# Kernel optimization log

Hardware: AMD Instinct MI355X
Metric: run time of the kernel (lower is better)

The kernel has to match this reference:

```python
import jax, jax.numpy as jnp
import numpy as np

EPS_BN = 1e-5

def _grid_sample(fea, gx, gy):
    # fea: [B,C,H,W]; gx,gy: [B,P] normalized to [-1,1]; bilinear, zeros padding, align_corners=True
    B, C, H, W = fea.shape
    x = (gx + 1.0) * 0.5 * (W - 1)
    y = (gy + 1.0) * 0.5 * (H - 1)
    x0 = jnp.floor(x)
    y0 = jnp.floor(y)
    wx1 = x - x0
    wy1 = y - y0
    flat = fea.reshape(B, C, H * W)
    def tap(xi, yi, w):
        valid = ((xi >= 0) & (xi <= W - 1) & (yi >= 0) & (yi <= H - 1)).astype(fea.dtype)
        xi_c = jnp.clip(xi, 0, W - 1).astype(jnp.int32)
        yi_c = jnp.clip(yi, 0, H - 1).astype(jnp.int32)
        g = jnp.take_along_axis(flat, (yi_c * W + xi_c)[:, None, :], axis=2)  # [B,C,P]
        return g * (w * valid)[:, None, :]
    return (tap(x0, y0, (1 - wx1) * (1 - wy1)) + tap(x0 + 1, y0, wx1 * (1 - wy1))
            + tap(x0, y0 + 1, (1 - wx1) * wy1) + tap(x0 + 1, y0 + 1, wx1 * wy1))

def _homo_warp(src_fea, src_proj, ref_proj, depth_values):
    # src_fea: [B,C,H,W] -> warped [B,C,D,H,W] (MVSNet homo_warping, grid under stop_gradient)
    B, C, H, W = src_fea.shape
    D = depth_values.shape[1]
    proj = jnp.matmul(src_proj, jnp.linalg.inv(ref_proj))
    rot, trans = proj[:, :3, :3], proj[:, :3, 3]
    yy, xx = jnp.meshgrid(jnp.arange(H, dtype=src_fea.dtype), jnp.arange(W, dtype=src_fea.dtype), indexing='ij')
    xyz = jnp.stack([xx.ravel(), yy.ravel(), jnp.ones(H * W, src_fea.dtype)], 0)  # [3,HW]
    rot_xyz = jnp.einsum('bij,jp->bip', rot, xyz)  # [B,3,HW]
    pxyz = rot_xyz[:, :, None, :] * depth_values.reshape(B, 1, D, H * W) + trans[:, :, None, None]  # [B,3,D,HW]
    z = pxyz[:, 2]
    gx = jax.lax.stop_gradient(((pxyz[:, 0] / z) / ((W - 1) / 2.0) - 1.0).reshape(B, D * H * W))
    gy = jax.lax.stop_gradient(((pxyz[:, 1] / z) / ((H - 1) / 2.0) - 1.0).reshape(B, D * H * W))
    return _grid_sample(src_fea, gx, gy).reshape(B, C, D, H, W)

def _pixelwise_net(x, w0, g0, b0, m0, v0, w1, g1, b1, m1, v1, w2, b2):
    # x: [B,1,D,H,W]; 1x1x1 Conv3d(bias=False)+BN+ReLU twice, then Conv3d(8->1)+sigmoid+max over D
    def bnrelu(h, g, b, m, v):
        s = (1, -1, 1, 1, 1)
        return jax.nn.relu((h - m.reshape(s)) * (g / jnp.sqrt(v + EPS_BN)).reshape(s) + b.reshape(s))
    h = bnrelu(jnp.einsum('oc,bcdhw->bodhw', w0, x), g0, b0, m0, v0)
    h = bnrelu(jnp.einsum('oc,bcdhw->bodhw', w1, h), g1, b1, m1, v1)
    h = jnp.einsum('oc,bcdhw->bodhw', w2, h) + b2.reshape(1, -1, 1, 1, 1)
    out = jax.nn.sigmoid(h[:, 0])  # [B,D,H,W]
    return jnp.max(out, axis=1, keepdims=True)  # [B,1,H,W]

def _forward(features, proj_matrices, depth_values, num_depth,
             pw_w0, pw_g0, pw_b0, pw_m0, pw_v0, pw_w1, pw_g1, pw_b1, pw_m1, pw_v1, pw_w2, pw_b2,
             reg_w, reg_b):
    ref_fea = features[0]
    B, C, H, W = ref_fea.shape
    V = features.shape[0]
    D = num_depth
    def proj_new(p):  # p: [B,2,4,4] -> K @ E on top 3 rows
        top = jnp.matmul(p[:, 1, :3, :3], p[:, 0, :3, :4])
        return jnp.concatenate([top, p[:, 0, 3:4, :]], axis=1)
    ref_proj_new = proj_new(proj_matrices[:, 0])
    sim_sum = jnp.zeros((B, 1, D, H, W), ref_fea.dtype)
    w_sum = jnp.full((B, 1, 1, H, W), 1e-5, ref_fea.dtype)
    vw_list = []
    for i in range(1, V):  # small fixed loop over source views
        src_proj_new = proj_new(proj_matrices[:, i])
        warped = _homo_warp(features[i], src_proj_new, ref_proj_new, depth_values)
        sim = jnp.mean(warped * ref_fea[:, :, None], axis=1, keepdims=True)  # [B,1,D,H,W]
        vw = _pixelwise_net(sim, pw_w0, pw_g0, pw_b0, pw_m0, pw_v0, pw_w1, pw_g1, pw_b1, pw_m1, pw_v1, pw_w2, pw_b2)
        vw_list.append(vw)
        sim_sum = sim_sum + sim * vw[:, :, None]
        w_sum = w_sum + vw[:, :, None]
    similarity = sim_sum / w_sum
    cost_reg = jax.lax.conv_general_dilated(similarity, reg_w, (1, 1, 1), 'SAME',
                                            dimension_numbers=('NCDHW', 'OIDHW', 'NCDHW')) + reg_b.reshape(1, -1, 1, 1, 1)
    prob_volume = jax.nn.softmax(cost_reg[:, 0], axis=1)  # exp(log_softmax) == softmax
    idx = jnp.argmax(prob_volume, axis=1, keepdims=True)
    depth = jnp.take_along_axis(depth_values, idx, axis=1)[:, 0]  # WTA depth [B,H,W]
    conf = jnp.max(prob_volume, axis=1)
    view_weights = jnp.concatenate(vw_list, axis=1)
    return depth, conf, prob_volume, cost_reg, view_weights

def setup_inputs():
    key = jax.random.key(0)
    ks = jax.random.split(key, 20)
    B, V, C, H, W, D = 2, 5, 32, 128, 160, 32
    features = jax.random.normal(ks[0], (V, B, C, H, W), jnp.float32)
    K = np.eye(4, dtype=np.float32)
    K[0, 0] = 180.0; K[1, 1] = 180.0; K[0, 2] = W / 2.0; K[1, 2] = H / 2.0
    pm = np.zeros((B, V, 2, 4, 4), np.float32)
    for v in range(V):
        E = np.eye(4, dtype=np.float32)
        E[0, 3] = 10.0 * v  # horizontal baseline per source view
        pm[:, v, 0] = E
        pm[:, v, 1] = K
    depth_values = jnp.broadcast_to(jnp.linspace(425.0, 935.0, D, dtype=jnp.float32)[None, :, None, None], (B, D, H, W)) + 0.0
    rn = lambda k, s, sc=0.3: jax.random.normal(k, s, jnp.float32) * sc
    return {
        'features': features,
        'proj_matrices': jnp.asarray(pm),
        'depth_values': depth_values,
        'num_depth': D,
        'pw_w0': rn(ks[1], (16, 1)),
        'pw_g0': 1.0 + rn(ks[2], (16,), 0.1), 'pw_b0': rn(ks[3], (16,), 0.1),
        'pw_m0': rn(ks[4], (16,), 0.1), 'pw_v0': 1.0 + 0.5 * jax.random.uniform(ks[5], (16,)),
        'pw_w1': rn(ks[6], (8, 16)),
        'pw_g1': 1.0 + rn(ks[7], (8,), 0.1), 'pw_b1': rn(ks[8], (8,), 0.1),
        'pw_m1': rn(ks[9], (8,), 0.1), 'pw_v1': 1.0 + 0.5 * jax.random.uniform(ks[10], (8,)),
        'pw_w2': rn(ks[11], (1, 8)),
        'pw_b2': rn(ks[12], (1,), 0.1),
        'reg_w': rn(ks[13], (1, 1, 3, 3, 3), 0.1),
        'reg_b': rn(ks[14], (1,), 0.1),
    }

def reference(features, proj_matrices, depth_values, num_depth,
              pw_w0, pw_g0, pw_b0, pw_m0, pw_v0, pw_w1, pw_g1, pw_b1, pw_m1, pw_v1, pw_w2, pw_b2,
              reg_w, reg_b):
    return _forward(features, proj_matrices, depth_values, num_depth,
                    pw_w0, pw_g0, pw_b0, pw_m0, pw_v0, pw_w1, pw_g1, pw_b1, pw_m1, pw_v1, pw_w2, pw_b2,
                    reg_w, reg_b)
```

## Files before the change

### kernel.cpp

```cpp
#include <hip/hip_runtime.h>
#include <math.h>

#define BB 2
#define VV 5
#define CC 32
#define HH 128
#define WW 160
#define DD 32
#define HWp (HH*WW)
#define NV (VV-1)
#define PX 16
#define MAXSLOT 18

#define OFF_RT   0
#define OFF_PRM  96
#define OFF_FEAT 512
#define OFF_SIM  (OFF_FEAT + VV*BB*HWp*CC)
#define OFF_T    (OFF_SIM + BB*DD*HWp)
#define OFF_TAB  (OFF_T + 16)
#define OFF_FLAG (OFF_TAB + 17*16)

#define OUT_DEPTH 0
#define OUT_CONF  (BB*HWp)
#define OUT_PROB  (2*BB*HWp)
#define OUT_COST  (OUT_PROB + BB*DD*HWp)
#define OUT_VW    (OUT_COST + BB*DD*HWp)

#define ZI(d,k)     smemU[(d)*17 + (k)]
#define DEP(d,k)    smemU[(d)*17 + (k)]
#define REF(p,c)    smemU[544 + (p)*36 + (c)]
#define GT(v,p,i)   smemU[1120 + ((v)*16 + (p))*18 + (i)]
#define AY0(v,p)    smemU[2272 + (v)*16 + (p)]
#define AY1(v,p)    smemU[2336 + (v)*16 + (p)]
#define IR0(v,p)    smemI[2400 + (v)*16 + (p)]
#define IR1(v,p)    smemI[2464 + (v)*16 + (p)]
#define IXB(v,p)    smemI[2528 + (v)*16 + (p)]
#define ISL(v,p)    smemI[2592 + (v)*16 + (p)]
#define BADF        smemI[2656]
#define SIMG(v,d,p) smemU[544 + (((v)*32 + (d))*17 + (p))]

__device__ void build_proj(const float* proj, int b, int v, double M[4][4]) {
    const float* E = proj + (((b*VV + v)*2 + 0)*16);
    const float* K = proj + (((b*VV + v)*2 + 1)*16);
    for (int r = 0; r < 3; r++)
        for (int c = 0; c < 4; c++) {
            double s = 0.0;
            for (int k = 0; k < 3; k++) s += (double)K[r*4+k] * (double)E[k*4+c];
            M[r][c] = s;
        }
    for (int c = 0; c < 4; c++) M[3][c] = (double)E[12+c];
}

__device__ void inv4(const double M[4][4], double out[4][4]) {
    double a[4][8];
    for (int i = 0; i < 4; i++)
        for (int j = 0; j < 4; j++) { a[i][j] = M[i][j]; a[i][4+j] = (i == j) ? 1.0 : 0.0; }
    for (int col = 0; col < 4; col++) {
        int piv = col; double best = fabs(a[col][col]);
        for (int r = col+1; r < 4; r++) if (fabs(a[r][col]) > best) { best = fabs(a[r][col]); piv = r; }
        if (piv != col) for (int j = 0; j < 8; j++) { double t = a[col][j]; a[col][j] = a[piv][j]; a[piv][j] = t; }
        double dinv = 1.0 / a[col][col];
        for (int j = 0; j < 8; j++) a[col][j] *= dinv;
        for (int r = 0; r < 4; r++) {
            if (r == col) continue;
            double f = a[r][col];
            for (int j = 0; j < 8; j++) a[r][j] -= f * a[col][j];
        }
    }
    for (int i = 0; i < 4; i++) for (int j = 0; j < 4; j++) out[i][j] = a[i][4+j];
}

__device__ void setup_body(const float* __restrict__ proj,
    const float* __restrict__ w0, const float* __restrict__ g0, const float* __restrict__ b0,
    const float* __restrict__ m0, const float* __restrict__ v0,
    const float* __restrict__ w1, const float* __restrict__ g1, const float* __restrict__ b1,
    const float* __restrict__ m1, const float* __restrict__ v1,
    const float* __restrict__ w2, const float* __restrict__ b2,
    float* __restrict__ ws, int t,
    float* __restrict__ prmL, float* __restrict__ TL) {

    if (t < BB*NV) {
        int b = t / NV, v = 1 + (t % NV);
        double refM[4][4], inv[4][4], S[4][4];
        build_proj(proj, b, 0, refM);
        inv4(refM, inv);
        build_proj(proj, b, v, S);
        float* rt = ws + OFF_RT + (b*NV + (v-1))*12;
        for (int r = 0; r < 3; r++) {
            for (int c = 0; c < 3; c++) {
                double s = 0.0;
                for (int k = 0; k < 4; k++) s += S[r][k] * inv[k][c];
                rt[r*3 + c] = (float)s;
            }
            double s = 0.0;
            for (int k = 0; k < 4; k++) s += S[r][k] * inv[k][3];
            rt[9 + r] = (float)s;
        }
    }

    if (t < 16) {
        float sc = g0[t] / sqrtf(v0[t] + 1e-5f);
        prmL[t]      = w0[t] * sc;
        prmL[16 + t] = b0[t] - m0[t] * sc;
    }
    if (t >= 32 && t < 160) {
        int i = t - 32, q = i >> 4, o = i & 15;
        float sc = g1[q] / sqrtf(v1[q] + 1e-5f);
        prmL[32 + q*16 + o] = w1[q*16 + o] * sc;
    }
    if (t >= 160 && t < 168) {
        int q = t - 160;
        float sc = g1[q] / sqrtf(v1[q] + 1e-5f);
        prmL[160 + q] = b1[q] - m1[q] * sc;
        prmL[168 + q] = w2[q];
    }
    if (t == 176) prmL[176] = b2[0];
    __syncthreads();

    if (t < BB) {
        int ok = 1;
        for (int i = 0; i < NV; i++) {
            const float* ri = ws + OFF_RT + (t*NV + i)*12;
            ok &= (fabsf(ri[6])        < 1e-6f);
            ok &= (fabsf(ri[7])        < 1e-6f);
            ok &= (fabsf(ri[8] - 1.f)  < 1e-6f);
            ok &= (fabsf(ri[10])       < 1e-6f);
            ok &= (fabsf(ri[11])       < 1e-6f);
        }
        ws[OFF_FLAG + t] = ok ? 1.f : 0.f;
    }

    if (t == 0) {
        float tmp[16]; int nk = 0;
        for (int o = 0; o < 16; o++) {
            float a = prmL[o];
            if (a != 0.f) tmp[nk++] = -prmL[16+o] / a;
        }
        for (int i = 1; i < nk; i++) {
            float key = tmp[i]; int j = i-1;
            while (j >= 0 && tmp[j] > key) { tmp[j+1] = tmp[j]; j--; }
            tmp[j+1] = key;
        }
        for (int i = 0; i < 16; i++) TL[i] = (i < nk) ? tmp[i] : 3.4e38f;
    }
    __syncthreads();

    if (t < 17*8) {
        int seg = t >> 3, q = t & 7;
        float lo = (seg == 0)  ? -1e30f : TL[seg-1];
        float hi = (seg == 16) ?  1e30f : TL[seg];
        float smid;
        if (hi > 1e29f)       smid = lo + 1.f;
        else if (lo < -1e29f) smid = hi - 1.f;
        else                  smid = 0.5f*(lo + hi);
        float alpha = 0.f, beta = prmL[160+q];
        #pragma unroll
        for (int o = 0; o < 16; o++) {
            float a = prmL[o], c = prmL[16+o];
            if (a*smid + c > 0.f) {
                alpha += prmL[32+q*16+o]*a;
                beta  += prmL[32+q*16+o]*c;
            }
        }
        ws[OFF_TAB + seg*16 + q]     = alpha;
        ws[OFF_TAB + seg*16 + 8 + q] = beta;
    }
    if (t < 177) ws[OFF_PRM + t] = prmL[t];
    if (t < 16)  ws[OFF_T + t]   = TL[t];
}

__global__ __launch_bounds__(256) void transpose_setup_kernel(
    const float* __restrict__ fea, float* __restrict__ featT,
    const float* __restrict__ proj,
    const float* __restrict__ w0, const float* __restrict__ g0, const float* __restrict__ b0,
    const float* __restrict__ m0, const float* __restrict__ v0,
    const float* __restrict__ w1, const float* __restrict__ g1, const float* __restrict__ b1,
    const float* __restrict__ m1, const float* __restrict__ v1,
    const float* __restrict__ w2, const float* __restrict__ b2,
    float* __restrict__ ws) {
    __shared__ float prmL[177];
    __shared__ float TL[16];
    if (blockIdx.x == 0)
        setup_body(proj, w0, g0, b0, m0, v0, w1, g1, b1, m1, v1, w2, b2,
                   ws, threadIdx.x, prmL, TL);

    int t = blockIdx.x*256 + threadIdx.x;
    int w = t % WW;
    int h = (t / WW) % HH;
    int b = (t / (WW*HH)) % BB;
    int v = t / (WW*HH*BB);
    const float* src = fea + (size_t)((v*BB + b)*CC) * HWp + h*WW + w;
    float* dst = featT + (size_t)((v*BB + b)*HWp + h*WW + w) * CC;
    #pragma unroll
    for (int c = 0; c < CC; c += 4) {
        float4 q;
        q.x = src[(c+0)*HWp];
        q.y = src[(c+1)*HWp];
        q.z = src[(c+2)*HWp];
        q.w = src[(c+3)*HWp];
        *reinterpret_cast<float4*>(dst + c) = q;
    }
}

__device__ __forceinline__ float half_max(float v) {
    v = fmaxf(v, __shfl_xor(v, 1));
    v = fmaxf(v, __shfl_xor(v, 2));
    v = fmaxf(v, __shfl_xor(v, 4));
    v = fmaxf(v, __shfl_xor(v, 8));
    v = fmaxf(v, __shfl_xor(v, 16));
    return v;
}

__device__ __forceinline__ float dot32(const float* __restrict__ col,
                                       const float* __restrict__ refp) {
    float acc = 0.f;
    #pragma unroll
    for (int c = 0; c < CC; c += 4) {
        float4 a = *reinterpret_cast<const float4*>(col + c);
        float4 r = *reinterpret_cast<const float4*>(refp + c);
        acc = fmaf(a.w, r.w, fmaf(a.z, r.z, fmaf(a.y, r.y, fmaf(a.x, r.x, acc))));
    }
    return acc;
}

__device__ __forceinline__ void mlp_out(
    float s0, float s1, float s2, float s3,
    int d2, int b, int p,
    const float* __restrict__ tabL, const float* __restrict__ Tg,
    const float* __restrict__ prm,
    float* __restrict__ out, float* __restrict__ simout) {
    float T0 = Tg[0], T1 = Tg[1], T2 = Tg[2], T3 = Tg[3];
    float T4 = Tg[4], T5 = Tg[5], T6 = Tg[6], T7 = Tg[7];
    float T8 = Tg[8], T9 = Tg[9], T10 = Tg[10], T11 = Tg[11];
    float T12 = Tg[12], T13 = Tg[13], T14 = Tg[14], T15 = Tg[15];
    float wq0 = prm[168], wq1 = prm[169], wq2 = prm[170], wq3 = prm[171];
    float wq4 = prm[172], wq5 = prm[173], wq6 = prm[174], wq7 = prm[175];
    float p176 = prm[176];

    float sv[NV] = {s0, s1, s2, s3};
    float vw[NV];
    #pragma unroll
    for (int v = 0; v < NV; v++) {
        float s = sv[v];
        int seg = 0;
        seg += (s > T0);  seg += (s > T1);  seg += (s > T2);  seg += (s > T3);
        seg += (s > T4);  seg += (s > T5);  seg += (s > T6);  seg += (s > T7);
        seg += (s > T8);  seg += (s > T9);  seg += (s > T10); seg += (s > T11);
        seg += (s > T12); seg += (s > T13); seg += (s > T14); seg += (s > T15);
        const float* row = &tabL[seg << 4];
        float4 A0 = *reinterpret_cast<const float4*>(row);
        float4 A1 = *reinterpret_cast<const float4*>(row + 4);
        float4 B0 = *reinterpret_cast<const float4*>(row + 8);
        float4 B1 = *reinterpret_cast<const float4*>(row + 12);
        float h2v = p176;
        h2v = fmaf(wq0, fmaxf(fmaf(A0.x, s, B0.x), 0.f), h2v);
        h2v = fmaf(wq1, fmaxf(fmaf(A0.y, s, B0.y), 0.f), h2v);
        h2v = fmaf(wq2, fmaxf(fmaf(A0.z, s, B0.z), 0.f), h2v);
        h2v = fmaf(wq3, fmaxf(fmaf(A0.w, s, B0.w), 0.f), h2v);
        h2v = fmaf(wq4, fmaxf(fmaf(A1.x, s, B1.x), 0.f), h2v);
        h2v = fmaf(wq5, fmaxf(fmaf(A1.y, s, B1.y), 0.f), h2v);
        h2v = fmaf(wq6, fmaxf(fmaf(A1.z, s, B1.z), 0.f), h2v);
        h2v = fmaf(wq7, fmaxf(fmaf(A1.w, s, B1.w), 0.f), h2v);
        float m = half_max(h2v);
        vw[v] = 1.f/(1.f + __expf(-m));
    }

    if (d2 == 0) out[OUT_VW + (b*NV + 0)*HWp + p] = vw[0];
    if (d2 == 1) out[OUT_VW + (b*NV + 1)*HWp + p] = vw[1];
    if (d2 == 2) out[OUT_VW + (b*NV + 2)*HWp + p] = vw[2];
    if (d2 == 3) out[OUT_VW + (b*NV + 3)*HWp + p] = vw[3];

    float wsum = 1e-5f + vw[0] + vw[1] + vw[2] + vw[3];
    float ssum = s0*vw[0] + s1*vw[1] + s2*vw[2] + s3*vw[3];
    simout[(b*DD + d2)*HWp + p] = ssum / wsum;
}

__device__ __forceinline__ float tap_blend(
    const float* __restrict__ vbv, int sub8, float sx,
    float ay0, float ay1, int r0, int r1,
    float4 rva, float4 rvb) {
    float x0f = floorf(sx);
    float wx1 = sx - x0f;
    float wx0 = 1.f - wx1;
    int xi0 = (int)x0f, xi1 = xi0 + 1;
    float ax0 = ((unsigned)xi0 < WW) ? wx0 : 0.f;
    float ax1 = ((unsigned)xi1 < WW) ? wx1 : 0.f;
    int xc0 = min(max(xi0, 0), WW-1);
    int xc1 = min(max(xi1, 0), WW-1);
    float w00 = ax0*ay0, w01 = ax1*ay0;
    const float* q00 = vbv + (((r0 + xc0) << 5) + sub8);
    const float* q01 = vbv + (((r0 + xc1) << 5) + sub8);
    float4 t00a = *reinterpret_cast<const float4*>(q00);
    float4 t00b = *reinterpret_cast<const float4*>(q00 + 4);
    float4 t01a = *reinterpret_cast<const float4*>(q01);
    float4 t01b = *reinterpret_cast<const float4*>(q01 + 4);

    float blx = fmaf(w01, t01a.x, w00*t00a.x);
    float bly = fmaf(w01, t01a.y, w00*t00a.y);
    float blz = fmaf(w01, t01a.z, w00*t00a.z);
    float blw = fmaf(w01, t01a.w, w00*t00a.w);
    float acc = fmaf(rva.w,blw, fmaf(rva.z,blz, fmaf(rva.y,bly, rva.x*blx)));
    blx = fmaf(w01, t01b.x, w00*t00b.x);
    bly = fmaf(w01, t01b.y, w00*t00b.y);
    blz = fmaf(w01, t01b.z, w00*t00b.z);
    blw = fmaf(w01, t01b.w, w00*t00b.w);
    acc = fmaf(rvb.w,blw, fmaf(rvb.z,blz, fmaf(rvb.y,bly, fmaf(rvb.x,blx, acc))));

    if (ay1 != 0.f) {
        float w10 = ax0*ay1, w11 = ax1*ay1;
        const float* q10 = vbv + (((r1 + xc0) << 5) + sub8);
        const float* q11 = vbv + (((r1 + xc1) << 5) + sub8);
        float4 t10a = *reinterpret_cast<const float4*>(q10);
        float4 t10b = *reinterpret_cast<const float4*>(q10 + 4);
        float4 t11a = *reinterpret_cast<const float4*>(q11);
        float4 t11b = *reinterpret_cast<const float4*>(q11 + 4);
        float cx = fmaf(w11, t11a.x, w10*t10a.x);
        float cy = fmaf(w11, t11a.y, w10*t10a.y);
        float cz = fmaf(w11, t11a.z, w10*t10a.z);
        float cw = fmaf(w11, t11a.w, w10*t10a.w);
        acc = fmaf(rva.w,cw, fmaf(rva.z,cz, fmaf(rva.y,cy, fmaf(rva.x,cx, acc))));
        cx = fmaf(w11, t11b.x, w10*t10b.x);
        cy = fmaf(w11, t11b.y, w10*t10b.y);
        cz = fmaf(w11, t11b.z, w10*t10b.z);
        cw = fmaf(w11, t11b.w, w10*t10b.w);
        acc = fmaf(rvb.w,cw, fmaf(rvb.z,cz, fmaf(rvb.y,cy, fmaf(rvb.x,cx, acc))));
    }
    return acc;
}

__global__ __launch_bounds__(256) void fused_sim_kernel(
    const float* __restrict__ featT, const float* __restrict__ rtAll,
    const float* __restrict__ prm, const float* __restrict__ Tg,
    const float* __restrict__ tabG, const float* __restrict__ flagG,
    const float* __restrict__ depthv,
    float* __restrict__ simout, float* __restrict__ out) {
    __shared__ __align__(16) float smemU[2720];
    __shared__ __align__(16) float tabL[17*16];
    int* smemI = (int*)smemU;

    int t = threadIdx.x;
    int b = blockIdx.y;
    int pbase = blockIdx.x * PX;
    int hi  = pbase / WW;
    int wi0 = pbase % WW;
    float fy = (float)hi;

    bool fast = (flagG[b] != 0.f);

    {
        int di = t >> 4, k = t & 15;
        float dep0 = depthv[(b*DD + di)*HWp + pbase + k];
        float dep1 = depthv[(b*DD + di + 16)*HWp + pbase + k];
        if (fast) {
            ZI(di, k)    = __builtin_amdgcn_rcpf(dep0);
            ZI(di+16, k) = __builtin_amdgcn_rcpf(dep1);
            if (t < 128) {
                int p = t >> 3, c4 = (t & 7) * 4;
                float4 rq = *reinterpret_cast<const float4*>(
                    featT + (size_t)(b*HWp + pbase + p)*CC + c4);
                *reinterpret_cast<float4*>(&REF(p, c4)) = rq;
            }
        } else {
            DEP(di, k)    = dep0;
            DEP(di+16, k) = dep1;
        }
        tabL[t] = tabG[t];
        if (t < 16) tabL[256 + t] = tabG[256 + t];
        if (t == 0 && fast) BADF = 0;
    }
    __syncthreads();

    float rc[NV][12];
    #pragma unroll
    for (int v = 0; v < NV; v++)
        #pragma unroll
        for (int j = 0; j < 12; j++)
            rc[v][j] = rtAll[(b*NV + v)*12 + j];
    float bx0[NV], by0[NV], bz0[NV];
    #pragma unroll
    for (int v = 0; v < NV; v++) {
        bx0[v] = fmaf((float)wi0, rc[v][0], fmaf(fy, rc[v][1], rc[v][2]));
        by0[v] = fmaf((float)wi0, rc[v][3], fmaf(fy, rc[v][4], rc[v][5]));
        bz0[v] = fmaf((float)wi0, rc[v][6], fmaf(fy, rc[v][7], rc[v][8]));
    }

    bool needRestage = false;
    if (fast) {
        int p_loc = t >> 5, d = t & 31;
        for (int ph = 0; ph < 2; ph++) {
            int p = ph*8 + p_loc;
            float zi = ZI(d, p);
            float mnz = zi, mxz = zi;
            #pragma unroll
            for (int off = 1; off <= 16; off <<= 1) {
                mnz = fminf(mnz, __shfl_xor(mnz, off));
                mxz = fmaxf(mxz, __shfl_xor(mxz, off));
            }
            if (d == 0) {
                float fk = (float)p;
                #pragma unroll
                for (int v = 0; v < NV; v++) {
                    float bx = fmaf(fk, rc[v][0], bx0[v]);
                    float t0c = rc[v][9];
                    float sxa = fmaf(t0c, mnz, bx);
                    float sxb = fmaf(t0c, mxz, bx);
                    float mn = fminf(sxa, sxb), mx = fmaxf(sxa, sxb);
                    float by = fmaf(fk, rc[v][3], by0[v]);
                    float sy = by;
                    float sny = rintf(sy);
                    sy = (fabsf(sy - sny) < 1e-4f) ? sny : sy;
                    float y0f = floorf(sy);
                    float wy1 = sy - y0f, wy0 = 1.f - wy1;
                    int yi0 = (int)y0f, yi1 = yi0 + 1;
                    AY0(v, p) = ((unsigned)yi0 < HH) ? wy0 : 0.f;
                    AY1(v, p) = ((unsigned)yi1 < HH) ? wy1 : 0.f;
                    IR0(v, p) = min(max(yi0, 0), HH-1)*WW;
                    IR1(v, p) = min(max(yi1, 0), HH-1)*WW;
                    bool finite = (mn > -1e9f) && (mx < 1e9f) && (mn == mn) && (mx == mx);
                    int xb = finite ? (int)floorf(mn) : 0;
                    int slots = finite ? ((int)floorf(mx) - xb + 2) : MAXSLOT + 1;
                    IXB(v, p) = xb;
                    ISL(v, p) = slots;
                    if (slots > MAXSLOT) BADF = 1;
                }
            }
        }
        __syncthreads();
        if (BADF) { fast = false; needRestage = true; }
    }

    if (fast) {
        {
            int v2 = t & 3, p2 = (t >> 2) & 15, i0 = t >> 6;
            float ay0 = AY0(v2, p2), ay1 = AY1(v2, p2);
            int r0 = IR0(v2, p2), r1 = IR1(v2, p2);
            int xb = IXB(v2, p2), slots = ISL(v2, p2);
            const float* vbv = featT + (size_t)(((v2+1)*BB + b)*HWp)*CC;
            const float* refp = &REF(p2, 0);
            for (int i2 = i0; i2 < slots; i2 += 4) {
                int xc = min(max(xb + i2, 0), WW-1);
                float g = ay0 * dot32(vbv + ((r0 + xc) << 5), refp);
                if (ay1 != 0.f) g = fmaf(ay1, dot32(vbv + ((r1 + xc) << 5), refp), g);
                GT(v2, p2, i2) = g * (1.f/(float)CC);
            }
        }
        __syncthreads();
        {
            int p_loc = t >> 5, d = t & 31;
            for (int ph = 0; ph < 2; ph++) {
                int p = ph*8 + p_loc;
                float fk = (float)p;
                float zi = ZI(d, p);
                float sv[NV];
                #pragma unroll
                for (int v = 0; v < NV; v++) {
                    float bx = fmaf(fk, rc[v][0], bx0[v]);
                    float sx = fmaf(rc[v][9], zi, bx);
                    float x0f = floorf(sx);
                    float wx1 = sx - x0f, wx0 = 1.f - wx1;
                    int xi0 = (int)x0f, xi1 = xi0 + 1;
                    float ax0 = ((unsigned)xi0 < WW) ? wx0 : 0.f;
                    float ax1 = ((unsigned)xi1 < WW) ? wx1 : 0.f;
                    int ii = xi0 - IXB(v, p);
                    float g0 = GT(v, p, ii);
                    float g1 = GT(v, p, ii+1);
                    sv[v] = fmaf(ax0, g0, ax1*g1);
                }
                mlp_out(sv[0], sv[1], sv[2], sv[3], d, b, pbase + p,
                        tabL, Tg, prm, out, simout);
            }
        }
        return;
    }

    if (needRestage) {
        int di = t >> 4, k = t & 15;
        DEP(di, k)    = depthv[(b*DD + di)*HWp + pbase + k];
        DEP(di+16, k) = depthv[(b*DD + di + 16)*HWp + pbase + k];
        __syncthreads();
    }
    {
        int sub = t & 3;
        int dB  = (t >> 2) & 31;
        int kk  = t >> 7;
        int sub8 = sub*8;
        #pragma unroll 2
        for (int j = 0; j < PX/2; j++) {
            int kpix = j*2 + kk;
            int p = pbase + kpix;
            float fk = (float)kpix;
            float depth = DEP(dB, kpix);
            const float* refp = featT + (size_t)(b*HWp + p)*CC + sub8;
            float4 rva = *reinterpret_cast<const float4*>(refp);
            float4 rvb = *reinterpret_cast<const float4*>(refp + 4);

            #pragma unroll
            for (int v = 0; v < NV; v++) {
                float bx = fmaf(fk, rc[v][0], bx0[v]);
                float by = fmaf(fk, rc[v][3], by0[v]);
                float bz = fmaf(fk, rc[v][6], bz0[v]);
                float px = fmaf(bx, depth, rc[v][9]);
                float py = fmaf(by, depth, rc[v][10]);
                float pz = fmaf(bz, depth, rc[v][11]);
                float zi = __builtin_amdgcn_rcpf(pz);
                float sx = px * zi, sy = py * zi;
                float sny = rintf(sy);
                sy = (fabsf(sy - sny) < 1e-4f) ? sny : sy;
                float y0f = floorf(sy);
                float wy1 = sy - y0f, wy0 = 1.f - wy1;
                int yi0 = (int)y0f, yi1 = yi0 + 1;
                float ay0 = ((unsigned)yi0 < HH) ? wy0 : 0.f;
                float ay1 = ((unsigned)yi1 < HH) ? wy1 : 0.f;
                int yc0 = min(max(yi0, 0), HH-1);
                int yc1 = min(max(yi1, 0), HH-1);
                int r0 = yc0*WW, r1 = yc1*WW;
                const float* vbv = featT + (size_t)(((v+1)*BB + b)*HWp)*CC;
                float acc = tap_blend(vbv, sub8, sx, ay0, ay1, r0, r1, rva, rvb);
                acc += __shfl_xor(acc, 1);
                acc += __shfl_xor(acc, 2);
                if (sub == 0) SIMG(v, dB, kpix) = acc * (1.f/(float)CC);
            }
        }
        __syncthreads();

        int p8 = t >> 5;
        int d2 = t & 31;
        #pragma unroll
        for (int pi = 0; pi < PX/8; pi++) {
            int pidx = pi*8 + p8;
            mlp_out(SIMG(0, d2, pidx), SIMG(1, d2, pidx),
                    SIMG(2, d2, pidx), SIMG(3, d2, pidx),
                    d2, b, pbase + pidx, tabL, Tg, prm, out, simout);
        }
    }
}

__global__ __launch_bounds__(256) void convsm_kernel(
    const float* __restrict__ sim, const float* __restrict__ rw,
    const float* __restrict__ rb, const float* __restrict__ depthv,
    float* __restrict__ out) {
    __shared__ float tile[34*121 + 7];
    int t = threadIdx.x;
    int tw = blockIdx.x * 8;
    int th = blockIdx.y * 8;
    int b  = blockIdx.z;

    for (int i = t; i < 34*120; i += 256) {
        int e = i / 120; int rem = i % 120;
        int h = rem / 12, w = rem % 12;
        int gd = e - 1, gh = th + h - 1, gw = tw + w - 1;
        float v = 0.f;
        if (w < 10 && gd >= 0 && gd < DD && (unsigned)gh < HH && (unsigned)gw < WW)
            v = sim[((b*DD + gd)*HH + gh)*WW + gw];
        tile[e*121 + rem] = v;
    }
    __syncthreads();

    float wk[27];
    #pragma unroll
    for (int i = 0; i < 27; i++) wk[i] = rw[i];
    float bias = rb[0];

    int p  = t >> 2, dq = t & 3;
    int ph = p >> 3, pw = p & 7;
    int d0 = dq * 8;

    float cost[8];
    #pragma unroll
    for (int j = 0; j < 8; j++) cost[j] = bias;
    #pragma unroll
    for (int e = 0; e < 10; e++) {
        int el = d0 + e;
        float s0 = 0.f, s1 = 0.f, s2 = 0.f;
        #pragma unroll
        for (int kh = 0; kh < 3; kh++) {
            #pragma unroll
            for (int kw = 0; kw < 3; kw++) {
                float x = tile[el*121 + (ph+kh)*12 + (pw+kw)];
                s0 = fmaf(wk[0*9 + kh*3 + kw], x, s0);
                s1 = fmaf(wk[1*9 + kh*3 + kw], x, s1);
                s2 = fmaf(wk[2*9 + kh*3 + kw], x, s2);
            }
        }
        if (e < 8)            cost[e]   += s0;
        if (e >= 1 && e <= 8) cost[e-1] += s1;
        if (e >= 2)           cost[e-2] += s2;
    }

    int pg = (th + ph)*WW + (tw + pw);
    #pragma unroll
    for (int j = 0; j < 8; j++)
        out[OUT_COST + (b*DD + d0 + j)*HWp + pg] = cost[j];

    float m = cost[0]; int mi = d0;
    #pragma unroll
    for (int j = 1; j < 8; j++) { if (cost[j] > m) { m = cost[j]; mi = d0 + j; } }
    #pragma unroll
    for (int off = 1; off <= 2; off <<= 1) {
        float m2 = __shfl_xor(m, off);
        int  i2 = __shfl_xor(mi, off);
        if (m2 > m || (m2 == m && i2 < mi)) { m = m2; mi = i2; }
    }
    float sum = 0.f;
    float e8[8];
    #pragma unroll
    for (int j = 0; j < 8; j++) { e8[j] = __expf(cost[j] - m); sum += e8[j]; }
    #pragma unroll
    for (int off = 1; off <= 2; off <<= 1) sum += __shfl_xor(sum, off);
    float inv = 1.f / sum;
    #pragma unroll
    for (int j = 0; j < 8; j++)
        out[OUT_PROB + (b*DD + d0 + j)*HWp + pg] = e8[j] * inv;
    if (dq == 0) {
        out[OUT_DEPTH + b*HWp + pg] = depthv[(b*DD + mi)*HWp + pg];
        out[OUT_CONF  + b*HWp + pg] = inv;
    }
}

extern "C" void kernel_launch(void* const* d_in, const int* in_sizes, int n_in,
                              void* d_out, int out_size, void* d_ws, size_t ws_size,
                              hipStream_t stream) {
    const float* features = (const float*)d_in[0];
    const float* proj     = (const float*)d_in[1];
    const float* depthv   = (const float*)d_in[2];
    const float* w0 = (const float*)d_in[4];
    const float* g0 = (const float*)d_in[5];
    const float* b0 = (const float*)d_in[6];
    const float* m0 = (const float*)d_in[7];
    const float* v0 = (const float*)d_in[8];
    const float* w1 = (const float*)d_in[9];
    const float* g1 = (const float*)d_in[10];
    const float* b1 = (const float*)d_in[11];
    const float* m1 = (const float*)d_in[12];
    const float* v1 = (const float*)d_in[13];
    const float* w2 = (const float*)d_in[14];
    const float* b2 = (const float*)d_in[15];
    const float* rw = (const float*)d_in[16];
    const float* rb = (const float*)d_in[17];
    float* out = (float*)d_out;
    float* ws  = (float*)d_ws;

    transpose_setup_kernel<<<VV*BB*HWp/256, 256, 0, stream>>>(
        features, ws + OFF_FEAT, proj,
        w0, g0, b0, m0, v0, w1, g1, b1, m1, v1, w2, b2, ws);

    fused_sim_kernel<<<dim3(HWp/PX, BB), 256, 0, stream>>>(
        ws + OFF_FEAT, ws + OFF_RT, ws + OFF_PRM, ws + OFF_T, ws + OFF_TAB,
        ws + OFF_FLAG, depthv, ws + OFF_SIM, out);

    convsm_kernel<<<dim3(WW/8, HH/8, BB), 256, 0, stream>>>(
        ws + OFF_SIM, rw, rb, depthv, out);
}
```

Before: 77.53 us.

## Stage shared source-view row segment in LDS when all pixels hit one row

Adds a uniform-row fast path. When every pixel in a block samples the same single source row per view (no second y tap), the union x-range of feature columns is loaded cooperatively into padded LDS once. The per-pixel dot products then read from LDS instead of issuing redundant global loads for overlapping columns. In exchange, LDS use per block grows by about 24KB, which may reduce occupancy, and an extra barrier and a reduction step are added.

```diff
diff --git a/kernel.cpp b/kernel.cpp
--- a/kernel.cpp
+++ b/kernel.cpp
@@ -11,6 +11,7 @@
 #define NV (VV-1)
 #define PX 16
 #define MAXSLOT 18
+#define UWMAX 44
 
 #define OFF_RT   0
 #define OFF_PRM  96
@@ -38,6 +39,10 @@
 #define ISL(v,p)    smemI[2592 + (v)*16 + (p)]
 #define BADF        smemI[2656]
 #define SIMG(v,d,p) smemU[544 + (((v)*32 + (d))*17 + (p))]
+#define COLU(v,ux,c) smemU[2720 + (v)*(UWMAX*33) + (ux)*33 + (c)]
+#define UOKI(v)     smemI[8528 + (v)]
+#define UXLOI(v)    smemI[8532 + (v)]
+#define UWI(v)      smemI[8536 + (v)]
 
 __device__ void build_proj(const float* proj, int b, int v, double M[4][4]) {
     const float* E = proj + (((b*VV + v)*2 + 0)*16);
@@ -219,6 +224,19 @@
         float4 a = *reinterpret_cast<const float4*>(col + c);
         float4 r = *reinterpret_cast<const float4*>(refp + c);
         acc = fmaf(a.w, r.w, fmaf(a.z, r.z, fmaf(a.y, r.y, fmaf(a.x, r.x, acc))));
+    }
+    return acc;
+}
+
+__device__ __forceinline__ float dot32_lds(const float* __restrict__ col,
+                                           const float* __restrict__ refp) {
+    float acc = 0.f;
+    #pragma unroll
+    for (int c = 0; c < CC; c += 4) {
+        acc = fmaf(col[c+3], refp[c+3],
+              fmaf(col[c+2], refp[c+2],
+              fmaf(col[c+1], refp[c+1],
+              fmaf(col[c+0], refp[c+0], acc))));
     }
     return acc;
 }
@@ -334,7 +352,7 @@
     const float* __restrict__ tabG, const float* __restrict__ flagG,
     const float* __restrict__ depthv,
     float* __restrict__ simout, float* __restrict__ out) {
-    __shared__ __align__(16) float smemU[2720];
+    __shared__ __align__(16) float smemU[8544];
     __shared__ __align__(16) float tabL[17*16];
     int* smemI = (int*)smemU;
 
@@ -429,22 +447,79 @@
         if (BADF) { fast = false; needRestage = true; }
     }
 
+    bool uni = false;
     if (fast) {
-        {
-            int v2 = t & 3, p2 = (t >> 2) & 15, i0 = t >> 6;
-            float ay0 = AY0(v2, p2), ay1 = AY1(v2, p2);
-            int r0 = IR0(v2, p2), r1 = IR1(v2, p2);
-            int xb = IXB(v2, p2), slots = ISL(v2, p2);
-            const float* vbv = featT + (size_t)(((v2+1)*BB + b)*HWp)*CC;
-            const float* refp = &REF(p2, 0);
-            for (int i2 = i0; i2 < slots; i2 += 4) {
-                int xc = min(max(xb + i2, 0), WW-1);
-                float g = ay0 * dot32(vbv + ((r0 + xc) << 5), refp);
-                if (ay1 != 0.f) g = fmaf(ay1, dot32(vbv + ((r1 + xc) << 5), refp), g);
-                GT(v2, p2, i2) = g * (1.f/(float)CC);
+        if (t < 64) {
+            int v = t >> 4, p = t & 15;
+            int ok = (AY1(v, p) == 0.f) && (IR0(v, p) == IR0(v, 0)) ? 1 : 0;
+            int xlo = IXB(v, p);
+            int xhi = xlo + ISL(v, p) - 1;
+            #pragma unroll
+            for (int off = 1; off <= 8; off <<= 1) {
+                ok  &= __shfl_xor(ok, off);
+                xlo  = min(xlo, __shfl_xor(xlo, off));
+                xhi  = max(xhi, __shfl_xor(xhi, off));
+            }
+            if (p == 0) {
+                int wdt = xhi - xlo + 1;
+                UOKI(v)  = (ok && wdt <= UWMAX) ? 1 : 0;
+                UXLOI(v) = xlo;
+                UWI(v)   = wdt;
             }
         }
         __syncthreads();
+        uni = UOKI(0) && UOKI(1) && UOKI(2) && UOKI(3);
+    }
+
+    if (fast) {
+        if (uni) {
+            for (int i = t; i < NV*UWMAX*8; i += 256) {
+                int v  = i / (UWMAX*8);
+                int rem = i - v*(UWMAX*8);
+                int ux = rem >> 3, c4 = (rem & 7) * 4;
+                if (ux < UWI(v)) {
+                    int xc = min(max(UXLOI(v) + ux, 0), WW-1);
+                    int r0 = IR0(v, 0);
+                    const float* src = featT + (size_t)(((v+1)*BB + b)*HWp)*CC
+                                       + ((r0 + xc) << 5) + c4;
+                    float4 q = *reinterpret_cast<const float4*>(src);
+                    COLU(v, ux, c4+0) = q.x;
+                    COLU(v, ux, c4+1) = q.y;
+                    COLU(v, ux, c4+2) = q.z;
+                    COLU(v, ux, c4+3) = q.w;
+                }
+            }
+            __syncthreads();
+            {
+                int v2 = t & 3, p2 = (t >> 2) & 15, i0 = t >> 6;
+                float ay0 = AY0(v2, p2);
+                int xb = IXB(v2, p2), slots = ISL(v2, p2);
+                int xoff = xb - UXLOI(v2);
+                const float* refp = &REF(p2, 0);
+                for (int i2 = i0; i2 < slots; i2 += 4) {
+                    const float* col = &COLU(v2, xoff + i2, 0);
+                    float g = ay0 * dot32_lds(col, refp);
+                    GT(v2, p2, i2) = g * (1.f/(float)CC);
+                }
+            }
+            __syncthreads();
+        } else {
+            {
+                int v2 = t & 3, p2 = (t >> 2) & 15, i0 = t >> 6;
+                float ay0 = AY0(v2, p2), ay1 = AY1(v2, p2);
+                int r0 = IR0(v2, p2), r1 = IR1(v2, p2);
+                int xb = IXB(v2, p2), slots = ISL(v2, p2);
+                const float* vbv = featT + (size_t)(((v2+1)*BB + b)*HWp)*CC;
+                const float* refp = &REF(p2, 0);
+                for (int i2 = i0; i2 < slots; i2 += 4) {
+                    int xc = min(max(xb + i2, 0), WW-1);
+                    float g = ay0 * dot32(vbv + ((r0 + xc) << 5), refp);
+                    if (ay1 != 0.f) g = fmaf(ay1, dot32(vbv + ((r1 + xc) << 5), refp), g);
+                    GT(v2, p2, i2) = g * (1.f/(float)CC);
+                }
+            }
+            __syncthreads();
+        }
         {
             int p_loc = t >> 5, d = t & 31;
             for (int ph = 0; ph < 2; ph++) {
```

After: 76.81 us. About the same (-0.9%).
